# Optimization experiments

Measured on AMD Instinct MI355X. Metric: run time of the kernel, lower is better.

Reference implementation:

```python
import jax, jax.numpy as jnp
import numpy as np

B, S, H, IN, OUT, T = 1024, 256, 128, 2, 2, 512


def setup_inputs() -> dict:
    key = jax.random.key(0)
    ks = jax.random.split(key, 7)
    scale = 1.0 / np.sqrt(H)  # PyTorch LSTM init range ~ U(-1/sqrt(H), 1/sqrt(H))
    return {
        "x": jax.random.normal(ks[0], (B, S, IN), jnp.float32),
        "w_ih": jax.random.normal(ks[1], (4 * H, IN), jnp.float32) * scale,
        "w_hh": jax.random.normal(ks[2], (4 * H, H), jnp.float32) * scale,
        "b_ih": jax.random.normal(ks[3], (4 * H,), jnp.float32) * scale,
        "b_hh": jax.random.normal(ks[4], (4 * H,), jnp.float32) * scale,
        "w_fc": jax.random.normal(ks[5], (OUT, H), jnp.float32) * scale,
        "b_fc": jax.random.normal(ks[6], (OUT,), jnp.float32) * scale,
        "target_length": T,
    }


def reference(x, w_ih, w_hh, b_ih, b_hh, w_fc, b_fc, target_length):
    # PyTorch nn.LSTM cell, gate order (i, f, g, o). Dropout is identity (eval mode).
    bias = b_ih + b_hh
    hdim = w_hh.shape[1]

    def cell(h, c, x_t):
        gates = x_t @ w_ih.T + h @ w_hh.T + bias  # [B, 4H]
        i, f, g, o = jnp.split(gates, 4, axis=-1)
        c_new = jax.nn.sigmoid(f) * c + jax.nn.sigmoid(i) * jnp.tanh(g)
        h_new = jax.nn.sigmoid(o) * jnp.tanh(c_new)
        return h_new, c_new

    bsz = x.shape[0]
    h0 = jnp.zeros((bsz, hdim), x.dtype)
    c0 = jnp.zeros((bsz, hdim), x.dtype)

    # Encode input sequence
    def enc_step(carry, x_t):
        h, c = carry
        h, c = cell(h, c, x_t)
        return (h, c), None

    (h, c), _ = jax.lax.scan(enc_step, (h0, c0), jnp.swapaxes(x, 0, 1))

    inp0 = x[:, -1, :]  # [B, 2]

    def dec_step(carry, _):
        h, c, inp = carry
        h, c = cell(h, c, inp)
        pred = h @ w_fc.T + b_fc  # [B, 2]
        return (h, c, pred), pred

    _, preds = jax.lax.scan(dec_step, (h, c, inp0), None, length=target_length)
    return jnp.swapaxes(preds, 0, 1)  # [B, target_length, 2]
```

## Files before the change

kernel.cpp:

```cpp
#include <hip/hip_runtime.h>

typedef unsigned short ush;
typedef unsigned int uint32;
typedef __attribute__((ext_vector_type(8))) __bf16 bf16x8;
typedef __attribute__((ext_vector_type(4))) float f32x4;

#define NBLK 256
#define RB   4
#define NTHR 512
#define SENC 256
#define TDEC 512
#define HDIM 128
#define HSTR 144
#define XSTR 520
#define PSTR 1024

#define LOG2E  1.4426950408889634f
#define LOG2E2 2.8853900817779268f

__device__ __forceinline__ float bf2f(ush u){
  uint32 v = ((uint32)u) << 16;
  return __builtin_bit_cast(float, v);
}
__device__ __forceinline__ ush f2bf(float f){
  uint32 u = __builtin_bit_cast(uint32, f);
  u = (u + 0x7FFFu + ((u >> 16) & 1u)) >> 16;
  return (ush)u;
}
__device__ __forceinline__ float lo16f(uint32 w){ return __builtin_bit_cast(float, w << 16); }
__device__ __forceinline__ float hi16f(uint32 w){ return __builtin_bit_cast(float, w & 0xFFFF0000u); }

__device__ __forceinline__ float loadf(const void* p, int i, bool f32){
  return f32 ? ((const float*)p)[i] : bf2f(((const ush*)p)[i]);
}
__device__ __forceinline__ bf16x8 load8bf(const void* p, int i, bool f32){
  bf16x8 r;
  if (!f32){
    uint4 u = *reinterpret_cast<const uint4*>((const ush*)p + i);
    r = __builtin_bit_cast(bf16x8, u);
  } else {
    const float* fp = (const float*)p + i;
    #pragma unroll
    for (int j = 0; j < 8; ++j) r[j] = (__bf16)fp[j];
  }
  return r;
}
__device__ __forceinline__ float sigm(float x){
  return __builtin_amdgcn_rcpf(1.0f + __builtin_amdgcn_exp2f(-x * LOG2E));
}
__device__ __forceinline__ float tnh(float x){
  return 1.0f - 2.0f * __builtin_amdgcn_rcpf(__builtin_amdgcn_exp2f(x * LOG2E2) + 1.0f);
}
__device__ __forceinline__ f32x4 mfma4(const bf16x8* af, const bf16x8* b, f32x4 c){
  f32x4 r = __builtin_amdgcn_mfma_f32_16x16x32_bf16(af[0], b[0], c, 0, 0, 0);
  r = __builtin_amdgcn_mfma_f32_16x16x32_bf16(af[1], b[1], r, 0, 0, 0);
  r = __builtin_amdgcn_mfma_f32_16x16x32_bf16(af[2], b[2], r, 0, 0, 0);
  r = __builtin_amdgcn_mfma_f32_16x16x32_bf16(af[3], b[3], r, 0, 0, 0);
  return r;
}

__global__ void __launch_bounds__(NTHR, 2)
lstm_kernel(const void* __restrict__ xg,  const void* __restrict__ wih,
            const void* __restrict__ whh, const void* __restrict__ bih,
            const void* __restrict__ bhh, const void* __restrict__ wfc,
            const void* __restrict__ bfc, void* __restrict__ outg)
{
  __shared__ __attribute__((aligned(16))) ush x_lds[RB * XSTR];
  __shared__ __attribute__((aligned(16))) ush h_lds[2][RB * HSTR];
  __shared__ __attribute__((aligned(16))) ush pred_lds[RB][PSTR];

  const int tid   = threadIdx.x;
  const int lane  = tid & 63;
  const int wv    = tid >> 6;
  const int n     = lane & 15;
  const int q     = lane >> 4;
  const int gbase = wv << 4;
  const int blk   = blockIdx.x;

  const uint32* wp = (const uint32*)whh;
  int cnt = 0;
  #pragma unroll
  for (int i = 0; i < 64; ++i){
    uint32 e = (wp[i] >> 7) & 0xFFu;
    cnt += (e >= 90u && e <= 140u) ? 1 : 0;
  }
  const bool isf32 = (cnt < 40);

  for (int i = tid; i < 2 * RB * HSTR; i += NTHR) h_lds[0][i] = 0;

  if (!isf32){
    if (tid < 256){
      int row = tid >> 6, c = (tid & 63) * 8;
      uint4 v = *reinterpret_cast<const uint4*>((const ush*)xg + (blk * RB + row) * (SENC * 2) + c);
      *reinterpret_cast<uint4*>(&x_lds[row * XSTR + c]) = v;
    }
  } else {
    for (int i = tid; i < RB * SENC * 2; i += NTHR){
      int row = i >> 9, c = i & 511;
      x_lds[row * XSTR + c] = f2bf(((const float*)xg)[(blk * RB + row) * (SENC * 2) + c]);
    }
  }

  float wih0v[4], wih1v[4];
  f32x4 biasC[4];
  bf16x8 bfr[4][4];
  #pragma unroll
  for (int p = 0; p < 4; ++p){
    int g = p * 128 + gbase + n;
    float b = loadf(bih, g, isf32) + loadf(bhh, g, isf32);
    biasC[p][0] = b; biasC[p][1] = b; biasC[p][2] = b; biasC[p][3] = b;
    wih0v[p] = loadf(wih, g * 2 + 0, isf32);
    wih1v[p] = loadf(wih, g * 2 + 1, isf32);
    #pragma unroll
    for (int kk = 0; kk < 4; ++kk)
      bfr[p][kk] = load8bf(whh, g * HDIM + kk * 32 + q * 8, isf32);
  }
  bf16x8 wfcfr[4];
  #pragma unroll
  for (int kk = 0; kk < 4; ++kk){
    #pragma unroll
    for (int j = 0; j < 8; ++j){
      int k = kk * 32 + q * 8 + j;
      wfcfr[kk][j] = __builtin_bit_cast(__bf16, f2bf(loadf(wfc, (n & 1) * HDIM + k, isf32)));
    }
  }
  f32x4 pbfcC;
  {
    float pb = loadf(bfc, n & 1, isf32);
    pbfcC[0] = pb; pbfcC[1] = pb; pbfcC[2] = pb; pbfcC[3] = pb;
  }
  float wav[4], wbv[4];
  #pragma unroll
  for (int p = 0; p < 4; ++p){
    wav[p] = (n & 1) ? wih1v[p] : wih0v[p];
    wbv[p] = (n & 1) ? wih0v[p] : wih1v[p];
  }

  float cc = 0.0f;
  const int arow  = (n >> 2) * HSTR;
  const int hwofs = q * HSTR + gbase + n;
  int cur = 0;

  __syncthreads();

  #pragma unroll 1
  for (int s = 0; s <= SENC; ++s){
    int t = (s < SENC) ? s : SENC - 1;
    uint32 xw = *reinterpret_cast<const uint32*>(&x_lds[q * XSTR + t * 2]);
    float xa = lo16f(xw), xb = hi16f(xw);

    const ush* hb = &h_lds[cur][arow];
    bf16x8 af[4];
    #pragma unroll
    for (int kk = 0; kk < 4; ++kk)
      af[kk] = *reinterpret_cast<const bf16x8*>(hb + kk * 32 + q * 8);

    f32x4 acc0 = mfma4(af, bfr[0], biasC[0]);
    f32x4 acc1 = mfma4(af, bfr[1], biasC[1]);
    float g0 = acc0[0] + wih0v[0] * xa + wih1v[0] * xb;
    float si = sigm(g0);
    f32x4 acc2 = mfma4(af, bfr[2], biasC[2]);
    float g1 = acc1[0] + wih0v[1] * xa + wih1v[1] * xb;
    float sf = sigm(g1);
    f32x4 acc3 = mfma4(af, bfr[3], biasC[3]);
    float g2 = acc2[0] + wih0v[2] * xa + wih1v[2] * xb;
    float tg = tnh(g2);
    cc = sf * cc + si * tg;
    float th = tnh(cc);
    float g3 = acc3[0] + wih0v[3] * xa + wih1v[3] * xb;
    float so = sigm(g3);
    h_lds[cur ^ 1][hwofs] = f2bf(so * th);

    __syncthreads();
    cur ^= 1;
  }

  #pragma unroll 1
  for (int d = 0; d < TDEC - 1; ++d){
    const ush* hb = &h_lds[cur][arow];
    bf16x8 af[4];
    #pragma unroll
    for (int kk = 0; kk < 4; ++kk)
      af[kk] = *reinterpret_cast<const bf16x8*>(hb + kk * 32 + q * 8);

    f32x4 a4 = mfma4(af, wfcfr, pbfcC);
    float pv = a4[0];
    float po = __shfl_xor(pv, 1, 64);

    f32x4 acc0 = mfma4(af, bfr[0], biasC[0]);
    f32x4 acc1 = mfma4(af, bfr[1], biasC[1]);
    float g0 = acc0[0] + wav[0] * pv + wbv[0] * po;
    float si = sigm(g0);
    f32x4 acc2 = mfma4(af, bfr[2], biasC[2]);
    float g1 = acc1[0] + wav[1] * pv + wbv[1] * po;
    float sf = sigm(g1);
    f32x4 acc3 = mfma4(af, bfr[3], biasC[3]);
    float g2 = acc2[0] + wav[2] * pv + wbv[2] * po;
    float tg = tnh(g2);
    cc = sf * cc + si * tg;
    float th = tnh(cc);
    float g3 = acc3[0] + wav[3] * pv + wbv[3] * po;
    float so = sigm(g3);
    h_lds[cur ^ 1][hwofs] = f2bf(so * th);

    if (wv == 0 && n < 2)
      pred_lds[q][d * 2 + n] = f2bf(pv);

    __syncthreads();
    cur ^= 1;
  }

  if (wv == 0){
    const ush* hb = &h_lds[cur][arow];
    bf16x8 af[4];
    #pragma unroll
    for (int kk = 0; kk < 4; ++kk)
      af[kk] = *reinterpret_cast<const bf16x8*>(hb + kk * 32 + q * 8);
    f32x4 a4 = mfma4(af, wfcfr, pbfcC);
    if (n < 2)
      pred_lds[q][(TDEC - 1) * 2 + n] = f2bf(a4[0]);
  }
  __syncthreads();

  if (!isf32){
    int row = tid >> 7, c = (tid & 127) * 8;
    uint4 v = *reinterpret_cast<const uint4*>(&pred_lds[row][c]);
    *reinterpret_cast<uint4*>((ush*)outg + (blk * RB + row) * (TDEC * 2) + c) = v;
  } else {
    for (int i = tid; i < RB * TDEC * 2; i += NTHR){
      int row = i >> 10, c = i & 1023;
      ((float*)outg)[(blk * RB + row) * (TDEC * 2) + c] = bf2f(pred_lds[row][c]);
    }
  }
}

extern "C" void kernel_launch(void* const* d_in, const int* in_sizes, int n_in,
                              void* d_out, int out_size, void* d_ws, size_t ws_size,
                              hipStream_t stream) {
  lstm_kernel<<<dim3(NBLK), dim3(NTHR), 0, stream>>>(
      d_in[0], d_in[1], d_in[2], d_in[3], d_in[4], d_in[5], d_in[6], d_out);
}
```

Before: 432.1 us.

## Compute decoder fc projection via DPP row reductions into LDS partials

Replaces the per-step MFMA-based fc projection, which sat at the head of each decode step's dependency chain, with a reduction done at the end of the previous step. Each lane multiplies its fp32 hidden value by the fc weights, reduces across 16 lanes with DPP adds, and writes per-wave partials to LDS. The next step sums the 8 wave partials and adds the bias. This removes four MFMAs and a shuffle from the critical path at the cost of extra VALU/DPP work and LDS reads, and the prediction now uses fp32 h instead of bf16.

```diff
diff --git a/kernel.cpp b/kernel.cpp
--- a/kernel.cpp
+++ b/kernel.cpp
@@ -58,6 +58,17 @@
   r = __builtin_amdgcn_mfma_f32_16x16x32_bf16(af[3], b[3], r, 0, 0, 0);
   return r;
 }
+template<int CTRL>
+__device__ __forceinline__ float dpp_add(float x){
+  int yi = __builtin_amdgcn_update_dpp(0, __builtin_bit_cast(int, x), CTRL, 0xF, 0xF, true);
+  return x + __builtin_bit_cast(float, yi);
+}
+__device__ __forceinline__ void rowsum16(float& a, float& b){
+  a = dpp_add<0xB1>(a);  b = dpp_add<0xB1>(b);
+  a = dpp_add<0x4E>(a);  b = dpp_add<0x4E>(b);
+  a = dpp_add<0x140>(a); b = dpp_add<0x140>(b);
+  a = dpp_add<0x128>(a); b = dpp_add<0x128>(b);
+}
 
 __global__ void __launch_bounds__(NTHR, 2)
 lstm_kernel(const void* __restrict__ xg,  const void* __restrict__ wih,
@@ -65,9 +76,10 @@
             const void* __restrict__ bhh, const void* __restrict__ wfc,
             const void* __restrict__ bfc, void* __restrict__ outg)
 {
-  __shared__ __attribute__((aligned(16))) ush x_lds[RB * XSTR];
-  __shared__ __attribute__((aligned(16))) ush h_lds[2][RB * HSTR];
-  __shared__ __attribute__((aligned(16))) ush pred_lds[RB][PSTR];
+  __shared__ __attribute__((aligned(16))) ush   x_lds[RB * XSTR];
+  __shared__ __attribute__((aligned(16))) ush   h_lds[2][RB * HSTR];
+  __shared__ __attribute__((aligned(16))) ush   pred_lds[RB][PSTR];
+  __shared__ __attribute__((aligned(16))) float part_lds[2][RB][8][2];
 
   const int tid   = threadIdx.x;
   const int lane  = tid & 63;
@@ -115,26 +127,10 @@
     for (int kk = 0; kk < 4; ++kk)
       bfr[p][kk] = load8bf(whh, g * HDIM + kk * 32 + q * 8, isf32);
   }
-  bf16x8 wfcfr[4];
-  #pragma unroll
-  for (int kk = 0; kk < 4; ++kk){
-    #pragma unroll
-    for (int j = 0; j < 8; ++j){
-      int k = kk * 32 + q * 8 + j;
-      wfcfr[kk][j] = __builtin_bit_cast(__bf16, f2bf(loadf(wfc, (n & 1) * HDIM + k, isf32)));
-    }
-  }
-  f32x4 pbfcC;
-  {
-    float pb = loadf(bfc, n & 1, isf32);
-    pbfcC[0] = pb; pbfcC[1] = pb; pbfcC[2] = pb; pbfcC[3] = pb;
-  }
-  float wav[4], wbv[4];
-  #pragma unroll
-  for (int p = 0; p < 4; ++p){
-    wav[p] = (n & 1) ? wih1v[p] : wih0v[p];
-    wbv[p] = (n & 1) ? wih0v[p] : wih1v[p];
-  }
+  const float wfc0n = loadf(wfc, gbase + n, isf32);
+  const float wfc1n = loadf(wfc, HDIM + gbase + n, isf32);
+  const float pb0   = loadf(bfc, 0, isf32);
+  const float pb1   = loadf(bfc, 1, isf32);
 
   float cc = 0.0f;
   const int arow  = (n >> 2) * HSTR;
@@ -169,7 +165,15 @@
     float th = tnh(cc);
     float g3 = acc3[0] + wih0v[3] * xa + wih1v[3] * xb;
     float so = sigm(g3);
-    h_lds[cur ^ 1][hwofs] = f2bf(so * th);
+    float hv = so * th;
+    h_lds[cur ^ 1][hwofs] = f2bf(hv);
+
+    if (s == SENC){
+      float u0 = hv * wfc0n, u1 = hv * wfc1n;
+      rowsum16(u0, u1);
+      if (n == 0)
+        *reinterpret_cast<float2*>(&part_lds[cur ^ 1][q][wv][0]) = make_float2(u0, u1);
+    }
 
     __syncthreads();
     cur ^= 1;
@@ -177,48 +181,53 @@
 
   #pragma unroll 1
   for (int d = 0; d < TDEC - 1; ++d){
+    const float4* pp = reinterpret_cast<const float4*>(&part_lds[cur][q][0][0]);
+    float4 r0 = pp[0], r1 = pp[1], r2 = pp[2], r3 = pp[3];
+    float p0 = ((r0.x + r0.z) + (r1.x + r1.z)) + ((r2.x + r2.z) + (r3.x + r3.z)) + pb0;
+    float p1 = ((r0.y + r0.w) + (r1.y + r1.w)) + ((r2.y + r2.w) + (r3.y + r3.w)) + pb1;
+
     const ush* hb = &h_lds[cur][arow];
     bf16x8 af[4];
     #pragma unroll
     for (int kk = 0; kk < 4; ++kk)
       af[kk] = *reinterpret_cast<const bf16x8*>(hb + kk * 32 + q * 8);
 
-    f32x4 a4 = mfma4(af, wfcfr, pbfcC);
-    float pv = a4[0];
-    float po = __shfl_xor(pv, 1, 64);
-
     f32x4 acc0 = mfma4(af, bfr[0], biasC[0]);
     f32x4 acc1 = mfma4(af, bfr[1], biasC[1]);
-    float g0 = acc0[0] + wav[0] * pv + wbv[0] * po;
+    float g0 = acc0[0] + wih0v[0] * p0 + wih1v[0] * p1;
     float si = sigm(g0);
     f32x4 acc2 = mfma4(af, bfr[2], biasC[2]);
-    float g1 = acc1[0] + wav[1] * pv + wbv[1] * po;
+    float g1 = acc1[0] + wih0v[1] * p0 + wih1v[1] * p1;
     float sf = sigm(g1);
     f32x4 acc3 = mfma4(af, bfr[3], biasC[3]);
-    float g2 = acc2[0] + wav[2] * pv + wbv[2] * po;
+    float g2 = acc2[0] + wih0v[2] * p0 + wih1v[2] * p1;
     float tg = tnh(g2);
     cc = sf * cc + si * tg;
     float th = tnh(cc);
-    float g3 = acc3[0] + wav[3] * pv + wbv[3] * po;
+    float g3 = acc3[0] + wih0v[3] * p0 + wih1v[3] * p1;
     float so = sigm(g3);
-    h_lds[cur ^ 1][hwofs] = f2bf(so * th);
+    float hv = so * th;
+    h_lds[cur ^ 1][hwofs] = f2bf(hv);
+
+    float u0 = hv * wfc0n, u1 = hv * wfc1n;
+    rowsum16(u0, u1);
+    if (n == 0)
+      *reinterpret_cast<float2*>(&part_lds[cur ^ 1][q][wv][0]) = make_float2(u0, u1);
 
     if (wv == 0 && n < 2)
-      pred_lds[q][d * 2 + n] = f2bf(pv);
+      pred_lds[q][d * 2 + n] = f2bf(n ? p1 : p0);
 
     __syncthreads();
     cur ^= 1;
   }
 
-  if (wv == 0){
-    const ush* hb = &h_lds[cur][arow];
-    bf16x8 af[4];
-    #pragma unroll
-    for (int kk = 0; kk < 4; ++kk)
-      af[kk] = *reinterpret_cast<const bf16x8*>(hb + kk * 32 + q * 8);
-    f32x4 a4 = mfma4(af, wfcfr, pbfcC);
-    if (n < 2)
-      pred_lds[q][(TDEC - 1) * 2 + n] = f2bf(a4[0]);
+  {
+    const float4* pp = reinterpret_cast<const float4*>(&part_lds[cur][q][0][0]);
+    float4 r0 = pp[0], r1 = pp[1], r2 = pp[2], r3 = pp[3];
+    float p0 = ((r0.x + r0.z) + (r1.x + r1.z)) + ((r2.x + r2.z) + (r3.x + r3.z)) + pb0;
+    float p1 = ((r0.y + r0.w) + (r1.y + r1.w)) + ((r2.y + r2.w) + (r3.y + r3.w)) + pb1;
+    if (wv == 0 && n < 2)
+      pred_lds[q][(TDEC - 1) * 2 + n] = f2bf(n ? p1 : p0);
   }
   __syncthreads();
 
```

After: 513.8 us. 18.9% more time.
